# Performance work log

Measured on AMD Instinct MI355X. Metric: run time of the kernel, lower is better.

## Reference

```python
import jax, jax.numpy as jnp
import numpy as np
from jax import lax

T, H, W, C, F = 8, 96, 160, 256, 256
KS = (3, 3, 3)


def setup_inputs() -> dict:
    key = jax.random.key(0)
    k1, k2, k3 = jax.random.split(key, 3)
    x = jax.random.normal(k1, (T, H, W, C), dtype=jnp.float32)
    # one [3,3,3,1,1] depthwise filter per channel, stacked along output axis -> [3,3,3,1,C]
    Wd = jax.random.normal(k2, KS + (1, C), dtype=jnp.float32) * 0.1
    # pointwise 1x1x1 conv weight [1,1,1,C,F] stored as [C,F]
    Wp = jax.random.normal(k3, (C, F), dtype=jnp.float32) * 0.1
    return {"x": x, "Wd": Wd, "Wp": Wp}


def reference(x, Wd, Wp):
    # expand_dims(axis=0): [1,T,H,W,C]
    cur = x[None]
    # depthwise 3D conv (the per-channel TF loop == grouped conv with groups=C)
    cur = lax.conv_general_dilated(
        cur, Wd,
        window_strides=(1, 1, 1),
        padding="SAME",
        dimension_numbers=("NDHWC", "DHWIO", "NDHWC"),
        feature_group_count=C,
    )
    # pointwise 1x1x1 conv == channel GEMM, fused with ReLU
    out = jax.nn.relu(jnp.einsum("bthwc,cf->bthwf", cur, Wp))
    # pool_size == (1,1,1) -> no pooling; squeeze(axis=0)
    return out[0]
```

## Files before the change

### kernel.cpp

```cpp
#include <hip/hip_runtime.h>
#include <hip/hip_bf16.h>

#define T_ 8
#define H_ 96
#define W_ 160
#define C_ 256
#define F_ 256
#define M_ (T_ * H_ * W_)

typedef __bf16 bf16_t;
typedef __bf16 bf16x2 __attribute__((ext_vector_type(2)));
typedef __bf16 bf16x8 __attribute__((ext_vector_type(8)));
typedef float  f32x2  __attribute__((ext_vector_type(2)));
typedef float  f32x4  __attribute__((ext_vector_type(4)));

__global__ void wp_transpose_kernel(const float* __restrict__ Wp,
                                    bf16_t* __restrict__ WpT) {
    int c = blockIdx.x;
    int f = threadIdx.x;
    WpT[f * C_ + c] = (bf16_t)Wp[c * F_ + f];
}


#define PLANE(I)                                                              \
  {                                                                           \
    const int hh = h0 + (I) - 1;                                              \
    f32x2 v[3][8];                                                            \
    _Pragma("unroll") for (int kw = 0; kw < 3; ++kw)                          \
      _Pragma("unroll") for (int tt = 0; tt < 8; ++tt) v[kw][tt] = f32x2{};   \
    if (hh >= 0 && hh < H_) {                              \
      const float* pb = x + (((long)hh * W_ + w) * C_ + c);                   \
      _Pragma("unroll") for (int tt = 0; tt < 8; ++tt)                        \
        v[1][tt] = *(const f32x2*)(pb + (long)tt * tstride);                  \
      if (hasL) {                                                             \
        _Pragma("unroll") for (int tt = 0; tt < 8; ++tt)                      \
          v[0][tt] = *(const f32x2*)(pb - C_ + (long)tt * tstride);           \
      }                                                                       \
      if (hasR) {                                                             \
        _Pragma("unroll") for (int tt = 0; tt < 8; ++tt)                      \
          v[2][tt] = *(const f32x2*)(pb + C_ + (long)tt * tstride);           \
      }                                                                       \
    }                                                                         \
    _Pragma("unroll") for (int kh = 0; kh < 3; ++kh) {                        \
      const int ko = (I) - kh;                      \
      if (ko >= 0 && ko <= 7) {                                               \
        _Pragma("unroll") for (int to = 0; to < 8; ++to) {                    \
          f32x2 sum = f32x2{};                                                \
          _Pragma("unroll") for (int kt = 0; kt < 3; ++kt) {                  \
            const int ti = to + kt - 1;                                       \
            if (ti >= 0 && ti < 8) {                                          \
              _Pragma("unroll") for (int kw = 0; kw < 3; ++kw)                \
                sum += v[kw][ti] * wreg[(kt * 3 + kh) * 3 + kw];              \
            }                                                                 \
          }                                                                   \
          if (kh == 0) acc[ko][to] = sum; else acc[ko][to] += sum;            \
        }                                                                     \
      }                                                                       \
    }                                                                         \
    const int kd = (I) - 2;                                                   \
    if (kd >= 0 && kd <= 7) {                                                 \
      _Pragma("unroll") for (int tt = 0; tt < 8; ++tt) {                      \
        bf16x2 o;                                                             \
        o[0] = (bf16_t)acc[kd][tt][0];                                        \
        o[1] = (bf16_t)acc[kd][tt][1];                                        \
        *(bf16x2*)&dw[(((long)tt * H_ + h0 + kd) * W_ + w) * C_ + c] = o;     \
      }                                                                       \
    }                                                                         \
  }

__global__ __launch_bounds__(128, 2) void dw_conv_kernel(const float* __restrict__ x,
                                                         const float* __restrict__ Wd,
                                                         bf16_t* __restrict__ dw) {
    int nchunk = gridDim.x >> 3;
    int bb  = (blockIdx.x & 7) * nchunk + (blockIdx.x >> 3);
    int hs  = bb / W_;
    int w   = bb % W_;
    int h0  = hs * 8;
    int tid = threadIdx.x;
    int c   = tid * 2;

    const bool hasL = (w > 0);
    const bool hasR = (w < W_ - 1);
    const int tstride = H_ * W_ * C_;

    f32x2 wreg[27];
#pragma unroll
    for (int k = 0; k < 27; ++k) wreg[k] = *(const f32x2*)&Wd[k * C_ + c];

    f32x2 acc[8][8];

    PLANE(0) PLANE(1) PLANE(2) PLANE(3) PLANE(4)
    PLANE(5) PLANE(6) PLANE(7) PLANE(8) PLANE(9)
}

#define BM 128
#define BN 128
#define BK 32
#define LDSTR 40

__global__ __launch_bounds__(256) void gemm_kernel(const bf16_t* __restrict__ A,
                                                   const bf16_t* __restrict__ Bt,
                                                   float* __restrict__ out) {
    __shared__ __align__(16) bf16_t As[BM * LDSTR];
    __shared__ __align__(16) bf16_t Bs[BN * LDSTR];

    int m0   = blockIdx.x * BM;
    int n0   = blockIdx.y * BN;
    int tid  = threadIdx.x;
    int lane = tid & 63;
    int wid  = tid >> 6;
    int wr   = wid >> 1;
    int wc   = wid & 1;
    int r16  = lane & 15;
    int kg   = lane >> 4;

    f32x4 acc[4][4] = {};

    for (int k0 = 0; k0 < C_; k0 += BK) {
        __syncthreads();
#pragma unroll
        for (int it = 0; it < 2; ++it) {
            int slot = tid + it * 256;
            int row  = slot >> 2;
            int seg  = slot & 3;
            uint4 va = *(const uint4*)&A[(long)(m0 + row) * C_ + k0 + seg * 8];
            *(uint4*)&As[row * LDSTR + seg * 8] = va;
            uint4 vb = *(const uint4*)&Bt[(n0 + row) * C_ + k0 + seg * 8];
            *(uint4*)&Bs[row * LDSTR + seg * 8] = vb;
        }
        __syncthreads();

        bf16x8 af[4], bfr[4];
#pragma unroll
        for (int m = 0; m < 4; ++m)
            af[m] = *(const bf16x8*)&As[(wr * 64 + m * 16 + r16) * LDSTR + kg * 8];
#pragma unroll
        for (int n = 0; n < 4; ++n)
            bfr[n] = *(const bf16x8*)&Bs[(wc * 64 + n * 16 + r16) * LDSTR + kg * 8];

#pragma unroll
        for (int m = 0; m < 4; ++m)
#pragma unroll
            for (int n = 0; n < 4; ++n)
                acc[m][n] = __builtin_amdgcn_mfma_f32_16x16x32_bf16(af[m], bfr[n], acc[m][n], 0, 0, 0);
    }

    int rbase = m0 + wr * 64 + kg * 4;
    int cbase = n0 + wc * 64 + r16;
#pragma unroll
    for (int m = 0; m < 4; ++m)
#pragma unroll
        for (int n = 0; n < 4; ++n)
#pragma unroll
            for (int r = 0; r < 4; ++r) {
                float v = acc[m][n][r];
                v = v > 0.f ? v : 0.f;
                out[(long)(rbase + m * 16 + r) * F_ + cbase + n * 16] = v;
            }
}

extern "C" void kernel_launch(void* const* d_in, const int* in_sizes, int n_in,
                              void* d_out, int out_size, void* d_ws, size_t ws_size,
                              hipStream_t stream) {
    const float* x  = (const float*)d_in[0];
    const float* Wd = (const float*)d_in[1];
    const float* Wp = (const float*)d_in[2];
    float* out = (float*)d_out;

    bf16_t* dw  = (bf16_t*)d_ws;
    bf16_t* WpT = (bf16_t*)((char*)d_ws + (size_t)M_ * C_ * 2);

    wp_transpose_kernel<<<C_, F_, 0, stream>>>(Wp, WpT);
    dw_conv_kernel<<<(H_ / 8) * W_, 128, 0, stream>>>(x, Wd, dw);
    gemm_kernel<<<dim3(M_ / BM, F_ / BN), 256, 0, stream>>>(dw, WpT, out);
}
```

Before: 117.0 us.

## Compute two output columns per thread in depthwise conv, stage weights in LDS

Each depthwise-conv block now produces two adjacent W columns, loading 4 input columns instead of 3 per output column. That lowers redundant global loads of overlapping neighbours and halves the grid. Filter weights move from 27 persistent registers into shared memory and are reloaded per kh, which frees registers for the doubled accumulator array (128 f32x2). The risks are higher register pressure at launch_bounds(128,2), possible spills, and fewer blocks for latency hiding.

```diff
diff --git a/kernel.cpp b/kernel.cpp
--- a/kernel.cpp
+++ b/kernel.cpp
@@ -21,49 +21,62 @@
     WpT[f * C_ + c] = (bf16_t)Wp[c * F_ + f];
 }
 
-
 #define PLANE(I)                                                              \
   {                                                                           \
     const int hh = h0 + (I) - 1;                                              \
-    f32x2 v[3][8];                                                            \
-    _Pragma("unroll") for (int kw = 0; kw < 3; ++kw)                          \
-      _Pragma("unroll") for (int tt = 0; tt < 8; ++tt) v[kw][tt] = f32x2{};   \
+    f32x2 v[4][8];                                                            \
+    _Pragma("unroll") for (int j = 0; j < 4; ++j)                             \
+      _Pragma("unroll") for (int tt = 0; tt < 8; ++tt) v[j][tt] = f32x2{};    \
     if (hh >= 0 && hh < H_) {                              \
-      const float* pb = x + (((long)hh * W_ + w) * C_ + c);                   \
+      const float* pb = x + (((long)hh * W_ + w0) * C_ + c);                  \
       _Pragma("unroll") for (int tt = 0; tt < 8; ++tt)                        \
         v[1][tt] = *(const f32x2*)(pb + (long)tt * tstride);                  \
+      _Pragma("unroll") for (int tt = 0; tt < 8; ++tt)                        \
+        v[2][tt] = *(const f32x2*)(pb + C_ + (long)tt * tstride);             \
       if (hasL) {                                                             \
         _Pragma("unroll") for (int tt = 0; tt < 8; ++tt)                      \
           v[0][tt] = *(const f32x2*)(pb - C_ + (long)tt * tstride);           \
       }                                                                       \
       if (hasR) {                                                             \
         _Pragma("unroll") for (int tt = 0; tt < 8; ++tt)                      \
-          v[2][tt] = *(const f32x2*)(pb + C_ + (long)tt * tstride);           \
+          v[3][tt] = *(const f32x2*)(pb + 2 * C_ + (long)tt * tstride);       \
       }                                                                       \
     }                                                                         \
     _Pragma("unroll") for (int kh = 0; kh < 3; ++kh) {                        \
       const int ko = (I) - kh;                      \
       if (ko >= 0 && ko <= 7) {                                               \
+        f32x2 wv[9];                                                          \
+        _Pragma("unroll") for (int kt = 0; kt < 3; ++kt)                      \
+          _Pragma("unroll") for (int kw = 0; kw < 3; ++kw)                    \
+            wv[kt * 3 + kw] =                                                 \
+                *(const f32x2*)&Ws[((kt * 3 + kh) * 3 + kw) * C_ + c];        \
         _Pragma("unroll") for (int to = 0; to < 8; ++to) {                    \
-          f32x2 sum = f32x2{};                                                \
+          f32x2 s0 = f32x2{}, s1 = f32x2{};                                   \
           _Pragma("unroll") for (int kt = 0; kt < 3; ++kt) {                  \
             const int ti = to + kt - 1;                                       \
             if (ti >= 0 && ti < 8) {                                          \
-              _Pragma("unroll") for (int kw = 0; kw < 3; ++kw)                \
-                sum += v[kw][ti] * wreg[(kt * 3 + kh) * 3 + kw];              \
+              _Pragma("unroll") for (int kw = 0; kw < 3; ++kw) {              \
+                s0 += v[kw][ti] * wv[kt * 3 + kw];                            \
+                s1 += v[kw + 1][ti] * wv[kt * 3 + kw];                        \
+              }                                                               \
             }                                                                 \
           }                                                                   \
-          if (kh == 0) acc[ko][to] = sum; else acc[ko][to] += sum;            \
+          if (kh == 0) { acc[ko][to][0] = s0; acc[ko][to][1] = s1; }          \
+          else         { acc[ko][to][0] += s0; acc[ko][to][1] += s1; }        \
         }                                                                     \
       }                                                                       \
     }                                                                         \
     const int kd = (I) - 2;                                                   \
     if (kd >= 0 && kd <= 7) {                                                 \
       _Pragma("unroll") for (int tt = 0; tt < 8; ++tt) {                      \
-        bf16x2 o;                                                             \
-        o[0] = (bf16_t)acc[kd][tt][0];                                        \
-        o[1] = (bf16_t)acc[kd][tt][1];                                        \
-        *(bf16x2*)&dw[(((long)tt * H_ + h0 + kd) * W_ + w) * C_ + c] = o;     \
+        bf16x2 o0, o1;                                                        \
+        o0[0] = (bf16_t)acc[kd][tt][0][0];                                    \
+        o0[1] = (bf16_t)acc[kd][tt][0][1];                                    \
+        o1[0] = (bf16_t)acc[kd][tt][1][0];                                    \
+        o1[1] = (bf16_t)acc[kd][tt][1][1];                                    \
+        bf16_t* pd = &dw[(((long)tt * H_ + h0 + kd) * W_ + w0) * C_ + c];     \
+        *(bf16x2*)pd = o0;                                                    \
+        *(bf16x2*)(pd + C_) = o1;                                             \
       }                                                                       \
     }                                                                         \
   }
@@ -71,23 +84,28 @@
 __global__ __launch_bounds__(128, 2) void dw_conv_kernel(const float* __restrict__ x,
                                                          const float* __restrict__ Wd,
                                                          bf16_t* __restrict__ dw) {
+    __shared__ float Ws[27 * C_];
+
+    for (int i = threadIdx.x; i < 27 * 64; i += 128) {
+        int k = i >> 6, q = i & 63;
+        *(f32x4*)&Ws[k * C_ + q * 4] = *(const f32x4*)&Wd[k * C_ + q * 4];
+    }
+    __syncthreads();
+
     int nchunk = gridDim.x >> 3;
     int bb  = (blockIdx.x & 7) * nchunk + (blockIdx.x >> 3);
-    int hs  = bb / W_;
-    int w   = bb % W_;
+    int hs  = bb / (W_ / 2);
+    int wp  = bb % (W_ / 2);
     int h0  = hs * 8;
+    int w0  = wp * 2;
     int tid = threadIdx.x;
     int c   = tid * 2;
 
-    const bool hasL = (w > 0);
-    const bool hasR = (w < W_ - 1);
+    const bool hasL = (w0 > 0);
+    const bool hasR = (w0 + 2 < W_);
     const int tstride = H_ * W_ * C_;
 
-    f32x2 wreg[27];
-#pragma unroll
-    for (int k = 0; k < 27; ++k) wreg[k] = *(const f32x2*)&Wd[k * C_ + c];
-
-    f32x2 acc[8][8];
+    f32x2 acc[8][8][2];
 
     PLANE(0) PLANE(1) PLANE(2) PLANE(3) PLANE(4)
     PLANE(5) PLANE(6) PLANE(7) PLANE(8) PLANE(9)
@@ -171,6 +189,6 @@
     bf16_t* WpT = (bf16_t*)((char*)d_ws + (size_t)M_ * C_ * 2);
 
     wp_transpose_kernel<<<C_, F_, 0, stream>>>(Wp, WpT);
-    dw_conv_kernel<<<(H_ / 8) * W_, 128, 0, stream>>>(x, Wd, dw);
+    dw_conv_kernel<<<(H_ / 8) * (W_ / 2), 128, 0, stream>>>(x, Wd, dw);
     gemm_kernel<<<dim3(M_ / BM, F_ / BN), 256, 0, stream>>>(dw, WpT, out);
 }
```

Measured after the change: 131.1 us. 12.1% more time.
